# Kernel tuning notes

Measured on AMD Instinct MI355X. Metric: run time of the kernel, lower is better.

The kernel has to match this reference:

```python
import jax, jax.numpy as jnp
import numpy as np

EPS = 1e-08


def setup_inputs() -> dict:
    key = jax.random.key(0)
    kx, ky = jax.random.split(key)
    x = jax.random.normal(kx, (8192, 512), dtype=jnp.float32)
    y = jax.random.normal(ky, (8192, 512), dtype=jnp.float32)
    return {"x": x, "y": y}


def reference(x, y):
    # Faithful to torch.nn.CosineSimilarity(dim=2, eps=EPS) applied to the
    # broadcast pair (x[i], y[j]):
    #   cos[i, j] = <x_i, y_j> / (max(||x_i||, eps) * max(||y_j||, eps))
    # Algebraically equivalent efficient form: normalize rows once, then GEMM.
    xn = x / jnp.maximum(jnp.linalg.norm(x, axis=1, keepdims=True), EPS)  # [Nx, L]
    yn = y / jnp.maximum(jnp.linalg.norm(y, axis=1, keepdims=True), EPS)  # [Ny, L]
    return jnp.einsum('il,jl->ij', xn, yn)  # [Nx, Ny]
```

## Files before the change

### kernel.cpp

```cpp
#include <hip/hip_runtime.h>


typedef __attribute__((ext_vector_type(8))) short bf16x8;
typedef __attribute__((ext_vector_type(4))) float f32x4;
typedef __attribute__((ext_vector_type(8))) unsigned short ushort8;

#define M_DIM 8192
#define N_DIM 8192
#define K_DIM 512

static __device__ __forceinline__ unsigned short f32_to_bf16(float f) {
  unsigned int u = __float_as_uint(f);
  u = (u + 0x7FFFu + ((u >> 16) & 1u)) >> 16;
  return (unsigned short)u;
}

__global__ __launch_bounds__(256) void normalize_rows(
    const float* __restrict__ in, unsigned short* __restrict__ out) {
  const int wid = threadIdx.x >> 6;
  const int lane = threadIdx.x & 63;
  const int row = (blockIdx.x << 2) + wid;
  const float4* r = (const float4*)(in + (size_t)row * K_DIM);
  float4 v0 = r[lane * 2];
  float4 v1 = r[lane * 2 + 1];
  float ss = v0.x * v0.x + v0.y * v0.y + v0.z * v0.z + v0.w * v0.w +
             v1.x * v1.x + v1.y * v1.y + v1.z * v1.z + v1.w * v1.w;
#pragma unroll
  for (int off = 32; off; off >>= 1) ss += __shfl_xor(ss, off, 64);
  const float s = 1.0f / fmaxf(sqrtf(ss), 1e-8f);
  const float f[8] = {v0.x, v0.y, v0.z, v0.w, v1.x, v1.y, v1.z, v1.w};
  union { ushort8 v; unsigned short u[8]; } o;
#pragma unroll
  for (int i = 0; i < 8; ++i) o.u[i] = f32_to_bf16(f[i] * s);
  *(ushort8*)(out + (size_t)row * K_DIM + lane * 8) = o.v;
}

static __device__ __forceinline__ void gl16(const unsigned short* g, char* l) {
  __builtin_amdgcn_global_load_lds(
      (const __attribute__((address_space(1))) unsigned int*)g,
      (__attribute__((address_space(3))) unsigned int*)l, 16, 0, 0);
}

#define BAR() __builtin_amdgcn_s_barrier()
#define SBAR() __builtin_amdgcn_sched_barrier(0)
#define LGKM0() do { asm volatile("s_waitcnt lgkmcnt(0)" ::: "memory"); \
                     __builtin_amdgcn_sched_barrier(0); } while (0)
#define VMCNT(n) do { asm volatile("s_waitcnt vmcnt(" #n ")" ::: "memory"); \
                      __builtin_amdgcn_sched_barrier(0); } while (0)

__global__ __launch_bounds__(512, 2) void cosgemm(
    const unsigned short* __restrict__ A,
    const unsigned short* __restrict__ B,
    float* __restrict__ C) {
  extern __shared__ char smem[];

  const int tid = threadIdx.x;
  const int lane = tid & 63;
  const int wid = tid >> 6;
  const int wm = wid >> 2;
  const int wn = wid & 3;
  const int lr16 = lane & 15;
  const int hq = lane >> 4;
  const int x7 = lane & 7;

  const int bid = blockIdx.x;
  const int L = bid >> 3;
  const int by = ((bid & 7) << 2) + (L & 3);
  const int bx = L >> 2;
  const int row0 = by << 8;
  const int col0 = bx << 8;

  const int rl = tid >> 3;
  const int sl = (tid & 7) ^ (rl & 7);
  const unsigned short* qA[2], * qB[2];
  qA[0] = A + (size_t)(row0 + rl) * K_DIM + sl * 8;
  qA[1] = A + (size_t)(row0 + 64 + rl) * K_DIM + sl * 8;
  qB[0] = B + (size_t)(col0 + rl) * K_DIM + sl * 8;
  qB[1] = B + (size_t)(col0 + 64 + rl) * K_DIM + sl * 8;

  auto stage = [&](int op, int half, int t) {
    const unsigned short* g0 = (op ? qB[0] : qA[0]) + half * 65536 + t * 64;
    const unsigned short* g1 = (op ? qB[1] : qA[1]) + half * 65536 + t * 64;
    char* l = smem + ((t & 1) << 16) + (op << 15) + (half << 14) + (wid << 10);
    gl16(g0, l);
    gl16(g1, l + 8192);
  };

  bf16x8 af[4][2], bf[4][2];
  f32x4 acc[8][4] = {};

  auto ldA = [&](int t, int fmBase) {
#pragma unroll
    for (int j = 0; j < 4; ++j) {
      const char* base = smem + ((t & 1) << 16) + (wm << 14) +
                         ((fmBase + j) * 16 + lr16) * 128;
#pragma unroll
      for (int kk = 0; kk < 2; ++kk)
        af[j][kk] = *(const bf16x8*)(base + ((((kk << 2) | hq) ^ x7) << 4));
    }
  };
  auto ldB = [&](int t, int fnBase) {
#pragma unroll
    for (int j = 0; j < 2; ++j) {
      const char* base = smem + ((t & 1) << 16) + 32768 + ((wn >> 1) << 14) +
                         (((wn & 1) << 6) + (fnBase + j) * 16 + lr16) * 128;
#pragma unroll
      for (int kk = 0; kk < 2; ++kk)
        bf[fnBase + j][kk] =
            *(const bf16x8*)(base + ((((kk << 2) | hq) ^ x7) << 4));
    }
  };
  auto mm = [&](int fmBase, int fnBase) {
    __builtin_amdgcn_s_setprio(1);
#pragma unroll
    for (int m = 0; m < 4; ++m)
#pragma unroll
      for (int n = 0; n < 2; ++n)
#pragma unroll
        for (int kk = 0; kk < 2; ++kk)
          acc[fmBase + m][fnBase + n] = __builtin_amdgcn_mfma_f32_16x16x32_bf16(
              af[m][kk], bf[fnBase + n][kk], acc[fmBase + m][fnBase + n], 0, 0, 0);
    __builtin_amdgcn_s_setprio(0);
  };

  stage(0, 0, 0); stage(0, 1, 0); stage(1, 0, 0); stage(1, 1, 0);
  stage(1, 0, 1); stage(1, 1, 1);
  VMCNT(4);
  BAR(); SBAR();

#pragma unroll
  for (int i = 0; i < 4; ++i) {
    const int t = 2 * i, u = 2 * i + 1;
    ldA(t, 0); ldB(t, 0); stage(0, 0, u);
    BAR(); LGKM0(); mm(0, 0); BAR();
    ldB(t, 2); stage(0, 1, u);
    BAR(); LGKM0(); mm(0, 2); BAR();
    ldA(t, 4); if (i < 3) stage(1, 0, t + 2);
    BAR(); LGKM0(); mm(4, 0); BAR();
    if (i < 3) stage(1, 1, t + 2);
    BAR(); LGKM0(); mm(4, 2);
    if (i < 3) { VMCNT(4); } else { VMCNT(0); }
    BAR(); SBAR();
    ldA(u, 0); ldB(u, 0); if (i < 3) stage(0, 0, t + 2);
    BAR(); LGKM0(); mm(0, 0); BAR();
    ldB(u, 2); if (i < 3) stage(0, 1, t + 2);
    BAR(); LGKM0(); mm(0, 2); BAR();
    ldA(u, 4); if (i < 3) stage(1, 0, t + 3);
    BAR(); LGKM0(); mm(4, 0); BAR();
    if (i < 3) stage(1, 1, t + 3);
    BAR(); LGKM0(); mm(4, 2);
    if (i < 3) { VMCNT(4); }
    BAR(); SBAR();
  }

  float* S = (float*)(smem + (wid << 13));
  const int crow0 = row0 + (wm << 7);
  const int ccol0 = col0 + (wn << 6);
#pragma unroll
  for (int fm = 0; fm < 8; ++fm) {
#pragma unroll
    for (int fn = 0; fn < 4; ++fn)
#pragma unroll
      for (int q = 0; q < 4; ++q)
        S[(hq * 4 + q) * 68 + fn * 16 + lr16] = acc[fm][fn][q];
#pragma unroll
    for (int j = 0; j < 4; ++j) {
      f32x4 v = *(const f32x4*)&S[(j * 4 + hq) * 68 + lr16 * 4];
      __builtin_nontemporal_store(
          v, (f32x4*)&C[(size_t)(crow0 + fm * 16 + j * 4 + hq) * N_DIM +
                        ccol0 + lr16 * 4]);
    }
  }
}

extern "C" void kernel_launch(void* const* d_in, const int* in_sizes, int n_in,
                              void* d_out, int out_size, void* d_ws, size_t ws_size,
                              hipStream_t stream) {
  const float* x = (const float*)d_in[0];
  const float* y = (const float*)d_in[1];
  float* out = (float*)d_out;
  unsigned short* xn = (unsigned short*)d_ws;
  unsigned short* yn = xn + (size_t)M_DIM * K_DIM;

  (void)hipFuncSetAttribute((const void*)cosgemm,
                            hipFuncAttributeMaxDynamicSharedMemorySize, 131072);

  normalize_rows<<<M_DIM / 4, 256, 0, stream>>>(x, xn);
  normalize_rows<<<N_DIM / 4, 256, 0, stream>>>(y, yn);
  cosgemm<<<(M_DIM / 256) * (N_DIM / 256), 512, 131072, stream>>>(xn, yn, out);
}
```

Baseline: 111.3 us.

## Make GEMM persistent over four column tiles and merge normalize launches

Each GEMM block now handles a 256x1024 strip: four 256x256 tiles computed in sequence, with the K-loop pipeline running straight across tile boundaries. The first three tiles are written straight from registers with scalar stores, and only the last one goes through the LDS-staged epilogue. The two normalize launches become one, and the grid shrinks from 1024 to 256 blocks. This is meant to cut launch overhead and pipeline prologue/drain costs, at the price of uncoalesced scalar stores for most tiles and fewer blocks to spread across CUs.

Result: slower. 138.0 us (+23.9%).

```diff
diff --git a/kernel.cpp b/kernel.cpp
--- a/kernel.cpp
+++ b/kernel.cpp
@@ -16,11 +16,14 @@
 }
 
 __global__ __launch_bounds__(256) void normalize_rows(
-    const float* __restrict__ in, unsigned short* __restrict__ out) {
+    const float* __restrict__ x, const float* __restrict__ y,
+    unsigned short* __restrict__ out) {
   const int wid = threadIdx.x >> 6;
   const int lane = threadIdx.x & 63;
   const int row = (blockIdx.x << 2) + wid;
-  const float4* r = (const float4*)(in + (size_t)row * K_DIM);
+  const float* src = row < M_DIM ? x + (size_t)row * K_DIM
+                                 : y + (size_t)(row - M_DIM) * K_DIM;
+  const float4* r = (const float4*)src;
   float4 v0 = r[lane * 2];
   float4 v1 = r[lane * 2 + 1];
   float ss = v0.x * v0.x + v0.y * v0.y + v0.z * v0.z + v0.w * v0.w +
@@ -64,11 +67,11 @@
   const int x7 = lane & 7;
 
   const int bid = blockIdx.x;
-  const int L = bid >> 3;
-  const int by = ((bid & 7) << 2) + (L & 3);
-  const int bx = L >> 2;
+  const int idx = bid >> 3;
+  const int by = ((bid & 7) << 2) + (idx & 3);
+  const int bxq = idx >> 2;
   const int row0 = by << 8;
-  const int col0 = bx << 8;
+  const int col0 = bxq << 10;
 
   const int rl = tid >> 3;
   const int sl = (tid & 7) ^ (rl & 7);
@@ -78,10 +81,10 @@
   qB[0] = B + (size_t)(col0 + rl) * K_DIM + sl * 8;
   qB[1] = B + (size_t)(col0 + 64 + rl) * K_DIM + sl * 8;
 
-  auto stage = [&](int op, int half, int t) {
-    const unsigned short* g0 = (op ? qB[0] : qA[0]) + half * 65536 + t * 64;
-    const unsigned short* g1 = (op ? qB[1] : qA[1]) + half * 65536 + t * 64;
-    char* l = smem + ((t & 1) << 16) + (op << 15) + (half << 14) + (wid << 10);
+  auto stage = [&](int op, int half, int par, size_t goff) {
+    const unsigned short* g0 = (op ? qB[0] : qA[0]) + goff + half * 65536;
+    const unsigned short* g1 = (op ? qB[1] : qA[1]) + goff + half * 65536;
+    char* l = smem + (par << 16) + (op << 15) + (half << 14) + (wid << 10);
     gl16(g0, l);
     gl16(g1, l + 8192);
   };
@@ -89,20 +92,20 @@
   bf16x8 af[4][2], bf[4][2];
   f32x4 acc[8][4] = {};
 
-  auto ldA = [&](int t, int fmBase) {
+  auto ldA = [&](int par, int fmBase) {
 #pragma unroll
     for (int j = 0; j < 4; ++j) {
-      const char* base = smem + ((t & 1) << 16) + (wm << 14) +
+      const char* base = smem + (par << 16) + (wm << 14) +
                          ((fmBase + j) * 16 + lr16) * 128;
 #pragma unroll
       for (int kk = 0; kk < 2; ++kk)
         af[j][kk] = *(const bf16x8*)(base + ((((kk << 2) | hq) ^ x7) << 4));
     }
   };
-  auto ldB = [&](int t, int fnBase) {
+  auto ldB = [&](int par, int fnBase) {
 #pragma unroll
     for (int j = 0; j < 2; ++j) {
-      const char* base = smem + ((t & 1) << 16) + 32768 + ((wn >> 1) << 14) +
+      const char* base = smem + (par << 16) + 32768 + ((wn >> 1) << 14) +
                          (((wn & 1) << 6) + (fnBase + j) * 16 + lr16) * 128;
 #pragma unroll
       for (int kk = 0; kk < 2; ++kk)
@@ -123,54 +126,84 @@
     __builtin_amdgcn_s_setprio(0);
   };
 
-  stage(0, 0, 0); stage(0, 1, 0); stage(1, 0, 0); stage(1, 1, 0);
-  stage(1, 0, 1); stage(1, 1, 1);
+  auto epi_direct = [&](int tau) {
+    const int crow0 = row0 + (wm << 7) + (hq << 2);
+    const int ccol0 = col0 + (tau << 8) + (wn << 6) + lr16;
+#pragma unroll
+    for (int fm = 0; fm < 8; ++fm)
+#pragma unroll
+      for (int fn = 0; fn < 4; ++fn)
+#pragma unroll
+        for (int q = 0; q < 4; ++q)
+          C[(size_t)(crow0 + fm * 16 + q) * N_DIM + ccol0 + (fn << 4)] =
+              acc[fm][fn][q];
+  };
+
+  auto epi_strip = [&](int tau) {
+    float* S = (float*)(smem + 32768 + (wid << 13));
+    const int crow0 = row0 + (wm << 7);
+    const int ccol0 = col0 + (tau << 8) + (wn << 6);
+#pragma unroll
+    for (int fm = 0; fm < 8; ++fm) {
+#pragma unroll
+      for (int fn = 0; fn < 4; ++fn)
+#pragma unroll
+        for (int q = 0; q < 4; ++q)
+          S[(hq * 4 + q) * 68 + fn * 16 + lr16] = acc[fm][fn][q];
+#pragma unroll
+      for (int r = 0; r < 4; ++r) {
+        f32x4 v = *(const f32x4*)&S[(r * 4 + hq) * 68 + lr16 * 4];
+        __builtin_nontemporal_store(
+            v, (f32x4*)&C[(size_t)(crow0 + fm * 16 + r * 4 + hq) * N_DIM +
+                          ccol0 + lr16 * 4]);
+      }
+    }
+  };
+
+  stage(0, 0, 0, 0); stage(0, 1, 0, 0);
+  stage(1, 0, 0, 0); stage(1, 1, 0, 0);
+  stage(1, 0, 1, 64); stage(1, 1, 1, 64);
   VMCNT(4);
   BAR(); SBAR();
 
-#pragma unroll
-  for (int i = 0; i < 4; ++i) {
-    const int t = 2 * i, u = 2 * i + 1;
-    ldA(t, 0); ldB(t, 0); stage(0, 0, u);
+#pragma unroll 1
+  for (int j = 0; j < 16; ++j) {
+    const bool st = (j < 15);
+    const int t2 = 2 * j + 2, t3 = 2 * j + 3;
+    const size_t gA_u = (size_t)((2 * j + 1) & 7) * 64;
+    const size_t gA_2 = (size_t)(t2 & 7) * 64;
+    const size_t gB_2 = (size_t)(t2 >> 3) * 131072 + (size_t)(t2 & 7) * 64;
+    const size_t gB_3 = (size_t)(t3 >> 3) * 131072 + (size_t)(t3 & 7) * 64;
+    ldA(0, 0); ldB(0, 0); stage(0, 0, 1, gA_u);
     BAR(); LGKM0(); mm(0, 0); BAR();
-    ldB(t, 2); stage(0, 1, u);
+    ldB(0, 2); stage(0, 1, 1, gA_u);
     BAR(); LGKM0(); mm(0, 2); BAR();
-    ldA(t, 4); if (i < 3) stage(1, 0, t + 2);
+    ldA(0, 4); if (st) stage(1, 0, 0, gB_2);
     BAR(); LGKM0(); mm(4, 0); BAR();
-    if (i < 3) stage(1, 1, t + 2);
+    if (st) stage(1, 1, 0, gB_2);
     BAR(); LGKM0(); mm(4, 2);
-    if (i < 3) { VMCNT(4); } else { VMCNT(0); }
+    if (st) { VMCNT(4); } else { VMCNT(0); }
     BAR(); SBAR();
-    ldA(u, 0); ldB(u, 0); if (i < 3) stage(0, 0, t + 2);
+    ldA(1, 0); ldB(1, 0); if (st) stage(0, 0, 0, gA_2);
     BAR(); LGKM0(); mm(0, 0); BAR();
-    ldB(u, 2); if (i < 3) stage(0, 1, t + 2);
+    ldB(1, 2); if (st) stage(0, 1, 0, gA_2);
     BAR(); LGKM0(); mm(0, 2); BAR();
-    ldA(u, 4); if (i < 3) stage(1, 0, t + 3);
+    ldA(1, 4); if (st) stage(1, 0, 1, gB_3);
     BAR(); LGKM0(); mm(4, 0); BAR();
-    if (i < 3) stage(1, 1, t + 3);
+    if (st) stage(1, 1, 1, gB_3);
     BAR(); LGKM0(); mm(4, 2);
-    if (i < 3) { VMCNT(4); }
+    if (st) { VMCNT(4); }
     BAR(); SBAR();
+    if ((j & 3) == 3 && j < 15) {
+      epi_direct(j >> 2);
+#pragma unroll
+      for (int fm = 0; fm < 8; ++fm)
+#pragma unroll
+        for (int fn = 0; fn < 4; ++fn)
+          acc[fm][fn] = (f32x4){0.f, 0.f, 0.f, 0.f};
+    }
   }
-
-  float* S = (float*)(smem + (wid << 13));
-  const int crow0 = row0 + (wm << 7);
-  const int ccol0 = col0 + (wn << 6);
-#pragma unroll
-  for (int fm = 0; fm < 8; ++fm) {
-#pragma unroll
-    for (int fn = 0; fn < 4; ++fn)
-#pragma unroll
-      for (int q = 0; q < 4; ++q)
-        S[(hq * 4 + q) * 68 + fn * 16 + lr16] = acc[fm][fn][q];
-#pragma unroll
-    for (int j = 0; j < 4; ++j) {
-      f32x4 v = *(const f32x4*)&S[(j * 4 + hq) * 68 + lr16 * 4];
-      __builtin_nontemporal_store(
-          v, (f32x4*)&C[(size_t)(crow0 + fm * 16 + j * 4 + hq) * N_DIM +
-                        ccol0 + lr16 * 4]);
-    }
-  }
+  epi_strip(3);
 }
 
 extern "C" void kernel_launch(void* const* d_in, const int* in_sizes, int n_in,
@@ -185,7 +218,6 @@
   (void)hipFuncSetAttribute((const void*)cosgemm,
                             hipFuncAttributeMaxDynamicSharedMemorySize, 131072);
 
-  normalize_rows<<<M_DIM / 4, 256, 0, stream>>>(x, xn);
-  normalize_rows<<<N_DIM / 4, 256, 0, stream>>>(y, yn);
-  cosgemm<<<(M_DIM / 256) * (N_DIM / 256), 512, 131072, stream>>>(xn, yn, out);
-}
+  normalize_rows<<<(M_DIM + N_DIM) / 4, 256, 0, stream>>>(x, y, xn);
+  cosgemm<<<256, 512, 131072, stream>>>(xn, yn, out);
+}
```

## Shrink GEMM tile to 256x128 with 4 waves, K-step 32, and fuse normalize launches

Applied to the files above, without the earlier changes.

Restructures the GEMM from a 256x256 tile with 8 waves and 64-wide K steps into a 256x128 tile with 4 waves and 32-wide K steps. LDS per block drops from 128KB to 48KB, and the staging swizzle and pipeline schedule are rewritten to match. The intent is to raise occupancy and double the number of blocks to improve load balance, at the cost of lower per-block data reuse and more barriers per unit of K. It also merges the two normalize launches into one to save a kernel launch.

After: 109.5 us. About the same (-1.7%).

```diff
diff --git a/kernel.cpp b/kernel.cpp
--- a/kernel.cpp
+++ b/kernel.cpp
@@ -16,11 +16,14 @@
 }
 
 __global__ __launch_bounds__(256) void normalize_rows(
-    const float* __restrict__ in, unsigned short* __restrict__ out) {
+    const float* __restrict__ x, const float* __restrict__ y,
+    unsigned short* __restrict__ out) {
   const int wid = threadIdx.x >> 6;
   const int lane = threadIdx.x & 63;
   const int row = (blockIdx.x << 2) + wid;
-  const float4* r = (const float4*)(in + (size_t)row * K_DIM);
+  const float* src = row < M_DIM ? x + (size_t)row * K_DIM
+                                 : y + (size_t)(row - M_DIM) * K_DIM;
+  const float4* r = (const float4*)src;
   float4 v0 = r[lane * 2];
   float4 v1 = r[lane * 2 + 1];
   float ss = v0.x * v0.x + v0.y * v0.y + v0.z * v0.z + v0.w * v0.w +
@@ -48,7 +51,7 @@
 #define VMCNT(n) do { asm volatile("s_waitcnt vmcnt(" #n ")" ::: "memory"); \
                       __builtin_amdgcn_sched_barrier(0); } while (0)
 
-__global__ __launch_bounds__(512, 2) void cosgemm(
+__global__ __launch_bounds__(256, 2) void cosgemm(
     const unsigned short* __restrict__ A,
     const unsigned short* __restrict__ B,
     float* __restrict__ C) {
@@ -57,57 +60,53 @@
   const int tid = threadIdx.x;
   const int lane = tid & 63;
   const int wid = tid >> 6;
-  const int wm = wid >> 2;
-  const int wn = wid & 3;
+  const int wm = wid >> 1;
+  const int wn = wid & 1;
   const int lr16 = lane & 15;
   const int hq = lane >> 4;
-  const int x7 = lane & 7;
+  const int sw = hq ^ (lr16 & 3);
 
   const int bid = blockIdx.x;
-  const int L = bid >> 3;
-  const int by = ((bid & 7) << 2) + (L & 3);
-  const int bx = L >> 2;
+  const int idx = bid >> 3;
+  const int by = ((bid & 7) << 2) + (idx & 3);
+  const int bx = idx >> 2;
   const int row0 = by << 8;
-  const int col0 = bx << 8;
+  const int col0 = bx << 7;
 
-  const int rl = tid >> 3;
-  const int sl = (tid & 7) ^ (rl & 7);
-  const unsigned short* qA[2], * qB[2];
-  qA[0] = A + (size_t)(row0 + rl) * K_DIM + sl * 8;
-  qA[1] = A + (size_t)(row0 + 64 + rl) * K_DIM + sl * 8;
-  qB[0] = B + (size_t)(col0 + rl) * K_DIM + sl * 8;
-  qB[1] = B + (size_t)(col0 + 64 + rl) * K_DIM + sl * 8;
+  const int srl = lane >> 2;
+  const int ssl = (lane & 3) ^ (srl & 3);
+  const unsigned short* pA =
+      A + (size_t)(row0 + (wid << 6) + srl) * K_DIM + ssl * 8;
+  const unsigned short* pB =
+      B + (size_t)(col0 + (wid << 5) + srl) * K_DIM + ssl * 8;
 
-  auto stage = [&](int op, int half, int t) {
-    const unsigned short* g0 = (op ? qB[0] : qA[0]) + half * 65536 + t * 64;
-    const unsigned short* g1 = (op ? qB[1] : qA[1]) + half * 65536 + t * 64;
-    char* l = smem + ((t & 1) << 16) + (op << 15) + (half << 14) + (wid << 10);
-    gl16(g0, l);
-    gl16(g1, l + 8192);
+  auto stageA2 = [&](int par, int cpair, int T) {
+    char* l = smem + par * 24576 + (wid << 12) + (cpair << 11);
+    const unsigned short* g = pA + T * 32 + (size_t)(cpair << 5) * K_DIM;
+    gl16(g, l);
+    gl16(g + (size_t)16 * K_DIM, l + 1024);
+  };
+  auto stageB1 = [&](int par, int c, int T) {
+    char* l = smem + par * 24576 + 16384 + (wid << 11) + (c << 10);
+    gl16(pB + T * 32 + (size_t)(c << 4) * K_DIM, l);
   };
 
-  bf16x8 af[4][2], bf[4][2];
+  bf16x8 af[4], bf[4];
   f32x4 acc[8][4] = {};
 
-  auto ldA = [&](int t, int fmBase) {
+  auto ldA = [&](int par, int fmBase) {
 #pragma unroll
     for (int j = 0; j < 4; ++j) {
-      const char* base = smem + ((t & 1) << 16) + (wm << 14) +
-                         ((fmBase + j) * 16 + lr16) * 128;
-#pragma unroll
-      for (int kk = 0; kk < 2; ++kk)
-        af[j][kk] = *(const bf16x8*)(base + ((((kk << 2) | hq) ^ x7) << 4));
+      const int row = (wm << 7) + (fmBase + j) * 16 + lr16;
+      af[j] = *(const bf16x8*)(smem + par * 24576 + row * 64 + (sw << 4));
     }
   };
-  auto ldB = [&](int t, int fnBase) {
+  auto ldB = [&](int par, int fnBase) {
 #pragma unroll
     for (int j = 0; j < 2; ++j) {
-      const char* base = smem + ((t & 1) << 16) + 32768 + ((wn >> 1) << 14) +
-                         (((wn & 1) << 6) + (fnBase + j) * 16 + lr16) * 128;
-#pragma unroll
-      for (int kk = 0; kk < 2; ++kk)
-        bf[fnBase + j][kk] =
-            *(const bf16x8*)(base + ((((kk << 2) | hq) ^ x7) << 4));
+      const int row = (wn << 6) + (fnBase + j) * 16 + lr16;
+      bf[fnBase + j] =
+          *(const bf16x8*)(smem + par * 24576 + 16384 + row * 64 + (sw << 4));
     }
   };
   auto mm = [&](int fmBase, int fnBase) {
@@ -116,44 +115,44 @@
     for (int m = 0; m < 4; ++m)
 #pragma unroll
       for (int n = 0; n < 2; ++n)
-#pragma unroll
-        for (int kk = 0; kk < 2; ++kk)
-          acc[fmBase + m][fnBase + n] = __builtin_amdgcn_mfma_f32_16x16x32_bf16(
-              af[m][kk], bf[fnBase + n][kk], acc[fmBase + m][fnBase + n], 0, 0, 0);
+        acc[fmBase + m][fnBase + n] = __builtin_amdgcn_mfma_f32_16x16x32_bf16(
+            af[m], bf[fnBase + n], acc[fmBase + m][fnBase + n], 0, 0, 0);
     __builtin_amdgcn_s_setprio(0);
   };
 
-  stage(0, 0, 0); stage(0, 1, 0); stage(1, 0, 0); stage(1, 1, 0);
-  stage(1, 0, 1); stage(1, 1, 1);
-  VMCNT(4);
+  stageA2(0, 0, 0); stageA2(0, 1, 0);
+  stageB1(0, 0, 0); stageB1(0, 1, 0);
+  stageB1(1, 0, 1); stageB1(1, 1, 1);
+  VMCNT(2);
   BAR(); SBAR();
 
-#pragma unroll
-  for (int i = 0; i < 4; ++i) {
-    const int t = 2 * i, u = 2 * i + 1;
-    ldA(t, 0); ldB(t, 0); stage(0, 0, u);
+#pragma unroll 1
+  for (int j = 0; j < 8; ++j) {
+    const bool st = (j < 7);
+    const int u = 2 * j + 1, t2 = 2 * j + 2, t3 = 2 * j + 3;
+    ldA(0, 0); ldB(0, 0); stageA2(1, 0, u);
     BAR(); LGKM0(); mm(0, 0); BAR();
-    ldB(t, 2); stage(0, 1, u);
+    ldB(0, 2); stageA2(1, 1, u);
     BAR(); LGKM0(); mm(0, 2); BAR();
-    ldA(t, 4); if (i < 3) stage(1, 0, t + 2);
+    ldA(0, 4); if (st) stageB1(0, 0, t2);
     BAR(); LGKM0(); mm(4, 0); BAR();
-    if (i < 3) stage(1, 1, t + 2);
+    if (st) stageB1(0, 1, t2);
     BAR(); LGKM0(); mm(4, 2);
-    if (i < 3) { VMCNT(4); } else { VMCNT(0); }
+    if (st) { VMCNT(2); } else { VMCNT(0); }
     BAR(); SBAR();
-    ldA(u, 0); ldB(u, 0); if (i < 3) stage(0, 0, t + 2);
+    ldA(1, 0); ldB(1, 0); if (st) stageA2(0, 0, t2);
     BAR(); LGKM0(); mm(0, 0); BAR();
-    ldB(u, 2); if (i < 3) stage(0, 1, t + 2);
+    ldB(1, 2); if (st) stageA2(0, 1, t2);
     BAR(); LGKM0(); mm(0, 2); BAR();
-    ldA(u, 4); if (i < 3) stage(1, 0, t + 3);
+    ldA(1, 4); if (st) stageB1(1, 0, t3);
     BAR(); LGKM0(); mm(4, 0); BAR();
-    if (i < 3) stage(1, 1, t + 3);
+    if (st) stageB1(1, 1, t3);
     BAR(); LGKM0(); mm(4, 2);
-    if (i < 3) { VMCNT(4); }
+    if (st) { VMCNT(2); }
     BAR(); SBAR();
   }
 
-  float* S = (float*)(smem + (wid << 13));
+  float* S = (float*)(smem + wid * 4352);
   const int crow0 = row0 + (wm << 7);
   const int ccol0 = col0 + (wn << 6);
 #pragma unroll
@@ -164,10 +163,10 @@
       for (int q = 0; q < 4; ++q)
         S[(hq * 4 + q) * 68 + fn * 16 + lr16] = acc[fm][fn][q];
 #pragma unroll
-    for (int j = 0; j < 4; ++j) {
-      f32x4 v = *(const f32x4*)&S[(j * 4 + hq) * 68 + lr16 * 4];
+    for (int r = 0; r < 4; ++r) {
+      f32x4 v = *(const f32x4*)&S[(r * 4 + hq) * 68 + lr16 * 4];
       __builtin_nontemporal_store(
-          v, (f32x4*)&C[(size_t)(crow0 + fm * 16 + j * 4 + hq) * N_DIM +
+          v, (f32x4*)&C[(size_t)(crow0 + fm * 16 + r * 4 + hq) * N_DIM +
                         ccol0 + lr16 * 4]);
     }
   }
@@ -183,9 +182,8 @@
   unsigned short* yn = xn + (size_t)M_DIM * K_DIM;
 
   (void)hipFuncSetAttribute((const void*)cosgemm,
-                            hipFuncAttributeMaxDynamicSharedMemorySize, 131072);
+                            hipFuncAttributeMaxDynamicSharedMemorySize, 65536);
 
-  normalize_rows<<<M_DIM / 4, 256, 0, stream>>>(x, xn);
-  normalize_rows<<<N_DIM / 4, 256, 0, stream>>>(y, yn);
-  cosgemm<<<(M_DIM / 256) * (N_DIM / 256), 512, 131072, stream>>>(xn, yn, out);
+  normalize_rows<<<(M_DIM + N_DIM) / 4, 256, 0, stream>>>(x, y, xn);
+  cosgemm<<<(M_DIM / 256) * (N_DIM / 128), 256, 49152, stream>>>(xn, yn, out);
 }
```
